# Kernel optimization log

Hardware: AMD Instinct MI355X
Metric: run time of the kernel (lower is better)

Reference implementation:

```python
import jax, jax.numpy as jnp
import numpy as np

# Circuit dimensions: B batch, N sum nodes (rows), C child nodes (cols), NSE stored edges.
B, N, C, NSE = 256, 8192, 32768, 524288


def setup_inputs() -> dict:
    key = jax.random.key(0)
    k1, k2, k3, k4 = jax.random.split(key, 4)
    # child log-likelihoods (output of child_layer.log_likelihood_of_nodes), [B, C]
    child_ll = jax.random.normal(k1, (B, C), dtype=jnp.float32) - 2.0
    # BCOO .data of the (unnormalized) log weights, [NSE]
    log_w_data = jax.random.normal(k2, (NSE,), dtype=jnp.float32)
    # BCOO indices[:, 0]: parent sum-node row of each edge. Guarantee every row
    # appears at least once so no node is empty (log(0) avoided), then sort
    # (matching .sort_indices() row-major ordering).
    rows = jnp.sort(jnp.concatenate([
        jnp.arange(N, dtype=jnp.int32),
        jax.random.randint(k3, (NSE - N,), 0, N, dtype=jnp.int32),
    ]))
    # BCOO indices[:, 1]: child node column of each edge
    cols = jax.random.randint(k4, (NSE,), 0, C, dtype=jnp.int32)
    return {"child_ll": child_ll, "log_w_data": log_w_data,
            "rows": rows, "cols": cols, "n_nodes": N}


def reference(child_ll, log_w_data, rows, cols, n_nodes):
    # log normalization constants per node (max-stabilized, as in
    # SparseSumLayer.log_normalization_constants)
    m = log_w_data.max()
    z = m + jnp.log(jax.ops.segment_sum(jnp.exp(log_w_data - m), rows,
                                        num_segments=n_nodes))  # [N]
    # per-edge: exp(log_w + child_ll[col])  (as in log_likelihood_of_nodes_single)
    vals = jnp.exp(log_w_data[None, :] + child_ll[:, cols])        # [B, NSE]
    # row-wise sparse sum (BCOO .sum(1).todense())
    summed = jax.ops.segment_sum(vals.T, rows, num_segments=n_nodes).T  # [B, N]
    # normalized log-likelihood of each sum node
    return jnp.log(summed) - z[None, :]
```

## Files before the change

kernel.cpp:

```cpp
#include <hip/hip_runtime.h>
#include <hip/hip_bf16.h>

#define BB   256
#define NN   8192
#define CC   32768
#define NSE_ 524288
#define GB   32
#define PREP_BLOCKS ((NSE_ + 64 + 255) / 256)
#define TP_BLOCKS   ((CC / 64) * 8)

typedef float v2f __attribute__((ext_vector_type(2)));

__device__ __forceinline__ unsigned int f2bf_rne(float f) {
    unsigned int u = __float_as_uint(f);
    return (u + 0x7fffu + ((u >> 16) & 1u)) >> 16;
}
__device__ __forceinline__ unsigned int pack2bf(float lo, float hi) {
    return f2bf_rne(lo) | (f2bf_rne(hi) << 16);
}

__global__ __launch_bounds__(256) void prep_transpose_kernel(
    const float* __restrict__ lw, const int* __restrict__ rows,
    const int* __restrict__ cols, const float* __restrict__ ll,
    uint2* __restrict__ cw, int* __restrict__ rs,
    unsigned int* __restrict__ cet32) {
    int bid = blockIdx.x;
    int t = threadIdx.x;
    if (bid < PREP_BLOCKS) {
        int e = bid * 256 + t;
        if (e < NSE_) {
            cw[e] = make_uint2((unsigned)cols[e],
                               __float_as_uint(__expf(lw[e])));
            if (e == 0) { rs[0] = 0; rs[NN] = NSE_; }
            else if (rows[e] != rows[e - 1]) rs[rows[e]] = e;
        } else if (e < NSE_ + 64) {
            cw[e] = make_uint2(0u, 0u);
        }
        return;
    }
    bid -= PREP_BLOCKS;
    int g = bid & 7;
    int ct = bid >> 3;
    int c0 = ct * 64, b0 = g * GB;
    __shared__ unsigned int tile_u[16][68];
    {
        int c4 = t & 15, bp = t >> 4;
        const float4 fa = *reinterpret_cast<const float4*>(
            ll + (size_t)(b0 + 2 * bp + 0) * CC + c0 + 4 * c4);
        const float4 fb = *reinterpret_cast<const float4*>(
            ll + (size_t)(b0 + 2 * bp + 1) * CC + c0 + 4 * c4);
        uint4 u;
        u.x = pack2bf(__expf(fa.x), __expf(fb.x));
        u.y = pack2bf(__expf(fa.y), __expf(fb.y));
        u.z = pack2bf(__expf(fa.z), __expf(fb.z));
        u.w = pack2bf(__expf(fa.w), __expf(fb.w));
        *reinterpret_cast<uint4*>(&tile_u[bp][4 * c4]) = u;
    }
    __syncthreads();
    {
        int c = t >> 2, q = t & 3;
        uint4 o;
        o.x = tile_u[4 * q + 0][c];
        o.y = tile_u[4 * q + 1][c];
        o.z = tile_u[4 * q + 2][c];
        o.w = tile_u[4 * q + 3][c];
        size_t base_u = ((size_t)g * CC + c0) * 16;
        *reinterpret_cast<uint4*>(cet32 + base_u + c * 16 + 4 * q) = o;
    }
}

__global__ __launch_bounds__(256) void sum_rows_kernel(
    const uint2* __restrict__ cw, const int* __restrict__ rs,
    const uint4* __restrict__ cet, float* __restrict__ out) {
    __shared__ uint2 stage[4][64];
    __shared__ float lds_out[32][17];
    int g = blockIdx.x & 7;
    int ntile = blockIdx.x >> 3;
    int n0 = ntile * 16;
    int wv = threadIdx.x >> 6;
    int lane = threadIdx.x & 63;
    int grp = lane >> 2;
    int bq = lane & 3;
    const uint4* slice = cet + (size_t)g * CC * 4;
    uint2* st = stage[wv];

    for (int r = 0; r < 4; ++r) {
        int n = n0 + wv * 4 + r;
        int s = __builtin_amdgcn_readfirstlane(rs[n]);
        int t = __builtin_amdgcn_readfirstlane(rs[n + 1]);
        v2f acc[4];
        acc[0] = 0.f; acc[1] = 0.f; acc[2] = 0.f; acc[3] = 0.f;
        float zs = 0.f;
        uint2 v = cw[s + lane];
        for (int eb = s; eb < t; eb += 64) {
            if (eb + lane >= t) v.y = 0u;
            st[lane] = v;
            if (eb + 64 < t) v = cw[eb + 64 + lane];
            #pragma unroll
            for (int j = 0; j < 4; ++j) {
                uint2 p = st[j * 16 + grp];
                float w = __uint_as_float(p.y);
                uint4 u = slice[(p.x << 2) | bq];
                v2f w2; w2.x = w; w2.y = w;
                v2f g0, g1, g2, g3;
                g0.x = __uint_as_float(u.x << 16);
                g0.y = __uint_as_float(u.x & 0xffff0000u);
                g1.x = __uint_as_float(u.y << 16);
                g1.y = __uint_as_float(u.y & 0xffff0000u);
                g2.x = __uint_as_float(u.z << 16);
                g2.y = __uint_as_float(u.z & 0xffff0000u);
                g3.x = __uint_as_float(u.w << 16);
                g3.y = __uint_as_float(u.w & 0xffff0000u);
                acc[0] += w2 * g0;
                acc[1] += w2 * g1;
                acc[2] += w2 * g2;
                acc[3] += w2 * g3;
                zs += w;
            }
        }
        #pragma unroll
        for (int off = 4; off <= 32; off <<= 1) {
            #pragma unroll
            for (int k = 0; k < 4; ++k) {
                acc[k].x += __shfl_xor(acc[k].x, off);
                acc[k].y += __shfl_xor(acc[k].y, off);
            }
            zs += __shfl_xor(zs, off);
        }
        if (grp == 0) {
            float lz = __logf(zs);
            #pragma unroll
            for (int k = 0; k < 4; ++k) {
                lds_out[bq * 8 + k * 2 + 0][wv * 4 + r] = __logf(acc[k].x) - lz;
                lds_out[bq * 8 + k * 2 + 1][wv * 4 + r] = __logf(acc[k].y) - lz;
            }
        }
    }
    __syncthreads();
    if (threadIdx.x < 128) {
        int bl = threadIdx.x >> 2, ch = threadIdx.x & 3;
        float4 v = make_float4(lds_out[bl][ch * 4 + 0], lds_out[bl][ch * 4 + 1],
                               lds_out[bl][ch * 4 + 2], lds_out[bl][ch * 4 + 3]);
        *reinterpret_cast<float4*>(
            out + (size_t)(g * GB + bl) * NN + n0 + ch * 4) = v;
    }
}

extern "C" void kernel_launch(void* const* d_in, const int* in_sizes, int n_in,
                              void* d_out, int out_size, void* d_ws, size_t ws_size,
                              hipStream_t stream) {
    const float* child_ll = (const float*)d_in[0];
    const float* log_w    = (const float*)d_in[1];
    const int*   rows     = (const int*)  d_in[2];
    const int*   cols     = (const int*)  d_in[3];
    float* out = (float*)d_out;

    char* ws = (char*)d_ws;
    uint2*        cwp = (uint2*)ws;
    int*          rs  = (int*)(ws + (size_t)6 * 1024 * 1024);
    unsigned int* cet = (unsigned int*)(ws + (size_t)8 * 1024 * 1024);

    prep_transpose_kernel<<<PREP_BLOCKS + TP_BLOCKS, 256, 0, stream>>>(
        log_w, rows, cols, child_ll, cwp, rs, cet);
    sum_rows_kernel<<<(NN / 16) * 8, 256, 0, stream>>>(
        cwp, rs, (const uint4*)cet, out);
}
```

Before: 128.1 us.

## Use persistent XCD-affine work stealing and interleave two rows per wave

Replaces the fixed block-to-(batch group, row tile) mapping with a persistent grid of 2048 blocks. Each block reads its XCD id and pulls row tiles through atomic counters, starting with the batch-group slice that matches its XCD so that slice stays hot in that XCD's L2. Each wave also processes two sum-node rows at once to expose more independent gathers. The costs are atomic and barrier overhead per tile, higher register pressure, and load imbalance when the two interleaved rows differ in length.

```diff
diff --git a/kernel.cpp b/kernel.cpp
--- a/kernel.cpp
+++ b/kernel.cpp
@@ -6,6 +6,7 @@
 #define CC   32768
 #define NSE_ 524288
 #define GB   32
+#define NTILES (NN / 16)
 #define PREP_BLOCKS ((NSE_ + 64 + 255) / 256)
 #define TP_BLOCKS   ((CC / 64) * 8)
 
@@ -23,10 +24,11 @@
     const float* __restrict__ lw, const int* __restrict__ rows,
     const int* __restrict__ cols, const float* __restrict__ ll,
     uint2* __restrict__ cw, int* __restrict__ rs,
-    unsigned int* __restrict__ cet32) {
+    unsigned int* __restrict__ cet32, int* __restrict__ cnt) {
     int bid = blockIdx.x;
     int t = threadIdx.x;
     if (bid < PREP_BLOCKS) {
+        if (bid == 0 && t < 8) cnt[t] = 0;
         int e = bid * 256 + t;
         if (e < NSE_) {
             cw[e] = make_uint2((unsigned)cols[e],
@@ -71,78 +73,126 @@
 
 __global__ __launch_bounds__(256) void sum_rows_kernel(
     const uint2* __restrict__ cw, const int* __restrict__ rs,
-    const uint4* __restrict__ cet, float* __restrict__ out) {
-    __shared__ uint2 stage[4][64];
+    const uint4* __restrict__ cet, int* __restrict__ cnt,
+    float* __restrict__ out) {
+    __shared__ uint2 stage[4][2][64];
     __shared__ float lds_out[32][17];
-    int g = blockIdx.x & 7;
-    int ntile = blockIdx.x >> 3;
-    int n0 = ntile * 16;
+    __shared__ int tile_sh;
     int wv = threadIdx.x >> 6;
     int lane = threadIdx.x & 63;
     int grp = lane >> 2;
     int bq = lane & 3;
-    const uint4* slice = cet + (size_t)g * CC * 4;
-    uint2* st = stage[wv];
-
-    for (int r = 0; r < 4; ++r) {
-        int n = n0 + wv * 4 + r;
-        int s = __builtin_amdgcn_readfirstlane(rs[n]);
-        int t = __builtin_amdgcn_readfirstlane(rs[n + 1]);
-        v2f acc[4];
-        acc[0] = 0.f; acc[1] = 0.f; acc[2] = 0.f; acc[3] = 0.f;
-        float zs = 0.f;
-        uint2 v = cw[s + lane];
-        for (int eb = s; eb < t; eb += 64) {
-            if (eb + lane >= t) v.y = 0u;
-            st[lane] = v;
-            if (eb + 64 < t) v = cw[eb + 64 + lane];
-            #pragma unroll
-            for (int j = 0; j < 4; ++j) {
-                uint2 p = st[j * 16 + grp];
-                float w = __uint_as_float(p.y);
-                uint4 u = slice[(p.x << 2) | bq];
-                v2f w2; w2.x = w; w2.y = w;
-                v2f g0, g1, g2, g3;
-                g0.x = __uint_as_float(u.x << 16);
-                g0.y = __uint_as_float(u.x & 0xffff0000u);
-                g1.x = __uint_as_float(u.y << 16);
-                g1.y = __uint_as_float(u.y & 0xffff0000u);
-                g2.x = __uint_as_float(u.z << 16);
-                g2.y = __uint_as_float(u.z & 0xffff0000u);
-                g3.x = __uint_as_float(u.w << 16);
-                g3.y = __uint_as_float(u.w & 0xffff0000u);
-                acc[0] += w2 * g0;
-                acc[1] += w2 * g1;
-                acc[2] += w2 * g2;
-                acc[3] += w2 * g3;
-                zs += w;
+    int xcd = __builtin_amdgcn_s_getreg(20 | (7 << 11)) & 7;
+
+    for (int k = 0; k < 8; ++k) {
+        int g = (xcd + k) & 7;
+        const uint4* slice = cet + (size_t)g * CC * 4;
+        for (;;) {
+            __syncthreads();
+            if (threadIdx.x == 0) tile_sh = atomicAdd(&cnt[g], 1);
+            __syncthreads();
+            int ntile = tile_sh;
+            if (ntile >= NTILES) break;
+            int n0 = ntile * 16;
+
+            for (int rp = 0; rp < 2; ++rp) {
+                int nA = n0 + wv * 4 + rp * 2;
+                int sA = __builtin_amdgcn_readfirstlane(rs[nA]);
+                int tA = __builtin_amdgcn_readfirstlane(rs[nA + 1]);
+                int sB = tA;
+                int tB = __builtin_amdgcn_readfirstlane(rs[nA + 2]);
+                v2f aA[4], aB[4];
+                aA[0] = 0.f; aA[1] = 0.f; aA[2] = 0.f; aA[3] = 0.f;
+                aB[0] = 0.f; aB[1] = 0.f; aB[2] = 0.f; aB[3] = 0.f;
+                float zA = 0.f, zB = 0.f;
+                uint2* stA = stage[wv][0];
+                uint2* stB = stage[wv][1];
+                uint2 vA = cw[sA + lane];
+                uint2 vB = cw[sB + lane];
+                int ebA = sA, ebB = sB;
+                while (ebA < tA || ebB < tB) {
+                    uint2 wA = vA, wB = vB;
+                    if (ebA + lane >= tA) wA.y = 0u;
+                    if (ebB + lane >= tB) wB.y = 0u;
+                    stA[lane] = wA;
+                    stB[lane] = wB;
+                    if (ebA + 64 < tA) vA = cw[ebA + 64 + lane];
+                    if (ebB + 64 < tB) vB = cw[ebB + 64 + lane];
+                    #pragma unroll
+                    for (int j = 0; j < 4; ++j) {
+                        uint2 pA = stA[j * 16 + grp];
+                        uint2 pB = stB[j * 16 + grp];
+                        uint4 uA = slice[(pA.x << 2) | bq];
+                        uint4 uB = slice[(pB.x << 2) | bq];
+                        float wa = __uint_as_float(pA.y);
+                        float wb = __uint_as_float(pB.y);
+                        v2f w2a; w2a.x = wa; w2a.y = wa;
+                        v2f w2b; w2b.x = wb; w2b.y = wb;
+                        v2f q0, q1, q2, q3;
+                        q0.x = __uint_as_float(uA.x << 16);
+                        q0.y = __uint_as_float(uA.x & 0xffff0000u);
+                        q1.x = __uint_as_float(uA.y << 16);
+                        q1.y = __uint_as_float(uA.y & 0xffff0000u);
+                        q2.x = __uint_as_float(uA.z << 16);
+                        q2.y = __uint_as_float(uA.z & 0xffff0000u);
+                        q3.x = __uint_as_float(uA.w << 16);
+                        q3.y = __uint_as_float(uA.w & 0xffff0000u);
+                        aA[0] += w2a * q0;
+                        aA[1] += w2a * q1;
+                        aA[2] += w2a * q2;
+                        aA[3] += w2a * q3;
+                        q0.x = __uint_as_float(uB.x << 16);
+                        q0.y = __uint_as_float(uB.x & 0xffff0000u);
+                        q1.x = __uint_as_float(uB.y << 16);
+                        q1.y = __uint_as_float(uB.y & 0xffff0000u);
+                        q2.x = __uint_as_float(uB.z << 16);
+                        q2.y = __uint_as_float(uB.z & 0xffff0000u);
+                        q3.x = __uint_as_float(uB.w << 16);
+                        q3.y = __uint_as_float(uB.w & 0xffff0000u);
+                        aB[0] += w2b * q0;
+                        aB[1] += w2b * q1;
+                        aB[2] += w2b * q2;
+                        aB[3] += w2b * q3;
+                        zA += wa;
+                        zB += wb;
+                    }
+                    ebA += 64;
+                    ebB += 64;
+                }
+                #pragma unroll
+                for (int off = 4; off <= 32; off <<= 1) {
+                    #pragma unroll
+                    for (int q = 0; q < 4; ++q) {
+                        aA[q].x += __shfl_xor(aA[q].x, off);
+                        aA[q].y += __shfl_xor(aA[q].y, off);
+                        aB[q].x += __shfl_xor(aB[q].x, off);
+                        aB[q].y += __shfl_xor(aB[q].y, off);
+                    }
+                    zA += __shfl_xor(zA, off);
+                    zB += __shfl_xor(zB, off);
+                }
+                if (grp == 0) {
+                    float lzA = __logf(zA), lzB = __logf(zB);
+                    int col = wv * 4 + rp * 2;
+                    #pragma unroll
+                    for (int q = 0; q < 4; ++q) {
+                        lds_out[bq * 8 + q * 2 + 0][col] = __logf(aA[q].x) - lzA;
+                        lds_out[bq * 8 + q * 2 + 1][col] = __logf(aA[q].y) - lzA;
+                        lds_out[bq * 8 + q * 2 + 0][col + 1] = __logf(aB[q].x) - lzB;
+                        lds_out[bq * 8 + q * 2 + 1][col + 1] = __logf(aB[q].y) - lzB;
+                    }
+                }
+            }
+            __syncthreads();
+            if (threadIdx.x < 128) {
+                int bl = threadIdx.x >> 2, ch = threadIdx.x & 3;
+                float4 v = make_float4(
+                    lds_out[bl][ch * 4 + 0], lds_out[bl][ch * 4 + 1],
+                    lds_out[bl][ch * 4 + 2], lds_out[bl][ch * 4 + 3]);
+                *reinterpret_cast<float4*>(
+                    out + (size_t)(g * GB + bl) * NN + n0 + ch * 4) = v;
             }
         }
-        #pragma unroll
-        for (int off = 4; off <= 32; off <<= 1) {
-            #pragma unroll
-            for (int k = 0; k < 4; ++k) {
-                acc[k].x += __shfl_xor(acc[k].x, off);
-                acc[k].y += __shfl_xor(acc[k].y, off);
-            }
-            zs += __shfl_xor(zs, off);
-        }
-        if (grp == 0) {
-            float lz = __logf(zs);
-            #pragma unroll
-            for (int k = 0; k < 4; ++k) {
-                lds_out[bq * 8 + k * 2 + 0][wv * 4 + r] = __logf(acc[k].x) - lz;
-                lds_out[bq * 8 + k * 2 + 1][wv * 4 + r] = __logf(acc[k].y) - lz;
-            }
-        }
-    }
-    __syncthreads();
-    if (threadIdx.x < 128) {
-        int bl = threadIdx.x >> 2, ch = threadIdx.x & 3;
-        float4 v = make_float4(lds_out[bl][ch * 4 + 0], lds_out[bl][ch * 4 + 1],
-                               lds_out[bl][ch * 4 + 2], lds_out[bl][ch * 4 + 3]);
-        *reinterpret_cast<float4*>(
-            out + (size_t)(g * GB + bl) * NN + n0 + ch * 4) = v;
     }
 }
 
@@ -158,10 +208,11 @@
     char* ws = (char*)d_ws;
     uint2*        cwp = (uint2*)ws;
     int*          rs  = (int*)(ws + (size_t)6 * 1024 * 1024);
+    int*          cnt = (int*)(ws + (size_t)7 * 1024 * 1024);
     unsigned int* cet = (unsigned int*)(ws + (size_t)8 * 1024 * 1024);
 
     prep_transpose_kernel<<<PREP_BLOCKS + TP_BLOCKS, 256, 0, stream>>>(
-        log_w, rows, cols, child_ll, cwp, rs, cet);
-    sum_rows_kernel<<<(NN / 16) * 8, 256, 0, stream>>>(
-        cwp, rs, (const uint4*)cet, out);
-}
+        log_w, rows, cols, child_ll, cwp, rs, cet, cnt);
+    sum_rows_kernel<<<2048, 256, 0, stream>>>(
+        cwp, rs, (const uint4*)cet, cnt, out);
+}
```

Result: slower. 337.3 us (+163.4%).

## Store exp child likelihoods as scaled FP8 and widen batch group to 64

Applied to the files above, without the earlier changes.

Converts the transposed exp(child_ll) table from bf16 to FP8, multiplied by a scale of 8 that is removed again in log space. Each 16-byte gather now yields 16 batch values instead of 8, so the batch group grows to 64 and the gather grid shrinks by half. This halves the random-gather traffic and the number of edge-list passes. In exchange, FP8 precision is much coarser, and small exp values can underflow, which risks accuracy failures.

```diff
diff --git a/kernel.cpp b/kernel.cpp
--- a/kernel.cpp
+++ b/kernel.cpp
@@ -5,25 +5,27 @@
 #define NN   8192
 #define CC   32768
 #define NSE_ 524288
-#define GB   32
+#define GB   64
 #define PREP_BLOCKS ((NSE_ + 64 + 255) / 256)
-#define TP_BLOCKS   ((CC / 64) * 8)
+#define TP_BLOCKS   ((CC / 64) * 4)
 
 typedef float v2f __attribute__((ext_vector_type(2)));
 
-__device__ __forceinline__ unsigned int f2bf_rne(float f) {
-    unsigned int u = __float_as_uint(f);
-    return (u + 0x7fffu + ((u >> 16) & 1u)) >> 16;
-}
-__device__ __forceinline__ unsigned int pack2bf(float lo, float hi) {
-    return f2bf_rne(lo) | (f2bf_rne(hi) << 16);
+#define FP8_SCALE  8.0f
+#define LOG_SCALE  2.0794415416798357f
+
+__device__ __forceinline__ unsigned int pack4_fp8(float a, float b, float c,
+                                                  float d) {
+    int v = __builtin_amdgcn_cvt_pk_fp8_f32(a, b, 0, false);
+    v = __builtin_amdgcn_cvt_pk_fp8_f32(c, d, v, true);
+    return (unsigned)v;
 }
 
 __global__ __launch_bounds__(256) void prep_transpose_kernel(
     const float* __restrict__ lw, const int* __restrict__ rows,
     const int* __restrict__ cols, const float* __restrict__ ll,
     uint2* __restrict__ cw, int* __restrict__ rs,
-    unsigned int* __restrict__ cet32) {
+    unsigned char* __restrict__ cet) {
     int bid = blockIdx.x;
     int t = threadIdx.x;
     if (bid < PREP_BLOCKS) {
@@ -39,33 +41,36 @@
         return;
     }
     bid -= PREP_BLOCKS;
-    int g = bid & 7;
-    int ct = bid >> 3;
+    int g = bid & 3;
+    int ct = bid >> 2;
     int c0 = ct * 64, b0 = g * GB;
-    __shared__ unsigned int tile_u[16][68];
-    {
-        int c4 = t & 15, bp = t >> 4;
-        const float4 fa = *reinterpret_cast<const float4*>(
-            ll + (size_t)(b0 + 2 * bp + 0) * CC + c0 + 4 * c4);
-        const float4 fb = *reinterpret_cast<const float4*>(
-            ll + (size_t)(b0 + 2 * bp + 1) * CC + c0 + 4 * c4);
-        uint4 u;
-        u.x = pack2bf(__expf(fa.x), __expf(fb.x));
-        u.y = pack2bf(__expf(fa.y), __expf(fb.y));
-        u.z = pack2bf(__expf(fa.z), __expf(fb.z));
-        u.w = pack2bf(__expf(fa.w), __expf(fb.w));
-        *reinterpret_cast<uint4*>(&tile_u[bp][4 * c4]) = u;
+    __shared__ float tile[64][65];
+    #pragma unroll
+    for (int k = 0; k < 4; ++k) {
+        int row = (t >> 4) + 16 * k;
+        int c4 = t & 15;
+        const float4 v = *reinterpret_cast<const float4*>(
+            ll + (size_t)(b0 + row) * CC + c0 + 4 * c4);
+        tile[c4 * 4 + 0][row] = v.x;
+        tile[c4 * 4 + 1][row] = v.y;
+        tile[c4 * 4 + 2][row] = v.z;
+        tile[c4 * 4 + 3][row] = v.w;
     }
     __syncthreads();
     {
-        int c = t >> 2, q = t & 3;
-        uint4 o;
-        o.x = tile_u[4 * q + 0][c];
-        o.y = tile_u[4 * q + 1][c];
-        o.z = tile_u[4 * q + 2][c];
-        o.w = tile_u[4 * q + 3][c];
-        size_t base_u = ((size_t)g * CC + c0) * 16;
-        *reinterpret_cast<uint4*>(cet32 + base_u + c * 16 + 4 * q) = o;
+        int cl = t >> 2, q = t & 3;
+        unsigned int o[4];
+        #pragma unroll
+        for (int i = 0; i < 4; ++i) {
+            int b = q * 16 + i * 4;
+            o[i] = pack4_fp8(__expf(tile[cl][b + 0]) * FP8_SCALE,
+                             __expf(tile[cl][b + 1]) * FP8_SCALE,
+                             __expf(tile[cl][b + 2]) * FP8_SCALE,
+                             __expf(tile[cl][b + 3]) * FP8_SCALE);
+        }
+        uint4 u4 = make_uint4(o[0], o[1], o[2], o[3]);
+        *reinterpret_cast<uint4*>(
+            cet + ((size_t)g * CC + c0 + cl) * GB + q * 16) = u4;
     }
 }
 
@@ -73,9 +78,9 @@
     const uint2* __restrict__ cw, const int* __restrict__ rs,
     const uint4* __restrict__ cet, float* __restrict__ out) {
     __shared__ uint2 stage[4][64];
-    __shared__ float lds_out[32][17];
-    int g = blockIdx.x & 7;
-    int ntile = blockIdx.x >> 3;
+    __shared__ float lds_out[64][17];
+    int g = blockIdx.x & 3;
+    int ntile = blockIdx.x >> 2;
     int n0 = ntile * 16;
     int wv = threadIdx.x >> 6;
     int lane = threadIdx.x & 63;
@@ -88,8 +93,9 @@
         int n = n0 + wv * 4 + r;
         int s = __builtin_amdgcn_readfirstlane(rs[n]);
         int t = __builtin_amdgcn_readfirstlane(rs[n + 1]);
-        v2f acc[4];
-        acc[0] = 0.f; acc[1] = 0.f; acc[2] = 0.f; acc[3] = 0.f;
+        v2f acc[8];
+        #pragma unroll
+        for (int k = 0; k < 8; ++k) acc[k] = 0.f;
         float zs = 0.f;
         uint2 v = cw[s + lane];
         for (int eb = s; eb < t; eb += 64) {
@@ -102,47 +108,43 @@
                 float w = __uint_as_float(p.y);
                 uint4 u = slice[(p.x << 2) | bq];
                 v2f w2; w2.x = w; w2.y = w;
-                v2f g0, g1, g2, g3;
-                g0.x = __uint_as_float(u.x << 16);
-                g0.y = __uint_as_float(u.x & 0xffff0000u);
-                g1.x = __uint_as_float(u.y << 16);
-                g1.y = __uint_as_float(u.y & 0xffff0000u);
-                g2.x = __uint_as_float(u.z << 16);
-                g2.y = __uint_as_float(u.z & 0xffff0000u);
-                g3.x = __uint_as_float(u.w << 16);
-                g3.y = __uint_as_float(u.w & 0xffff0000u);
-                acc[0] += w2 * g0;
-                acc[1] += w2 * g1;
-                acc[2] += w2 * g2;
-                acc[3] += w2 * g3;
+                acc[0] += w2 * __builtin_amdgcn_cvt_pk_f32_fp8(u.x, false);
+                acc[1] += w2 * __builtin_amdgcn_cvt_pk_f32_fp8(u.x, true);
+                acc[2] += w2 * __builtin_amdgcn_cvt_pk_f32_fp8(u.y, false);
+                acc[3] += w2 * __builtin_amdgcn_cvt_pk_f32_fp8(u.y, true);
+                acc[4] += w2 * __builtin_amdgcn_cvt_pk_f32_fp8(u.z, false);
+                acc[5] += w2 * __builtin_amdgcn_cvt_pk_f32_fp8(u.z, true);
+                acc[6] += w2 * __builtin_amdgcn_cvt_pk_f32_fp8(u.w, false);
+                acc[7] += w2 * __builtin_amdgcn_cvt_pk_f32_fp8(u.w, true);
                 zs += w;
             }
         }
         #pragma unroll
         for (int off = 4; off <= 32; off <<= 1) {
             #pragma unroll
-            for (int k = 0; k < 4; ++k) {
+            for (int k = 0; k < 8; ++k) {
                 acc[k].x += __shfl_xor(acc[k].x, off);
                 acc[k].y += __shfl_xor(acc[k].y, off);
             }
             zs += __shfl_xor(zs, off);
         }
         if (grp == 0) {
-            float lz = __logf(zs);
+            float lz = __logf(zs) + LOG_SCALE;
+            int col = wv * 4 + r;
             #pragma unroll
-            for (int k = 0; k < 4; ++k) {
-                lds_out[bq * 8 + k * 2 + 0][wv * 4 + r] = __logf(acc[k].x) - lz;
-                lds_out[bq * 8 + k * 2 + 1][wv * 4 + r] = __logf(acc[k].y) - lz;
+            for (int k = 0; k < 8; ++k) {
+                lds_out[bq * 16 + 2 * k + 0][col] = __logf(acc[k].x) - lz;
+                lds_out[bq * 16 + 2 * k + 1][col] = __logf(acc[k].y) - lz;
             }
         }
     }
     __syncthreads();
-    if (threadIdx.x < 128) {
+    {
         int bl = threadIdx.x >> 2, ch = threadIdx.x & 3;
-        float4 v = make_float4(lds_out[bl][ch * 4 + 0], lds_out[bl][ch * 4 + 1],
+        float4 o = make_float4(lds_out[bl][ch * 4 + 0], lds_out[bl][ch * 4 + 1],
                                lds_out[bl][ch * 4 + 2], lds_out[bl][ch * 4 + 3]);
         *reinterpret_cast<float4*>(
-            out + (size_t)(g * GB + bl) * NN + n0 + ch * 4) = v;
+            out + (size_t)(g * GB + bl) * NN + n0 + ch * 4) = o;
     }
 }
 
@@ -156,12 +158,12 @@
     float* out = (float*)d_out;
 
     char* ws = (char*)d_ws;
-    uint2*        cwp = (uint2*)ws;
-    int*          rs  = (int*)(ws + (size_t)6 * 1024 * 1024);
-    unsigned int* cet = (unsigned int*)(ws + (size_t)8 * 1024 * 1024);
+    uint2*         cwp = (uint2*)ws;
+    int*           rs  = (int*)(ws + (size_t)5 * 1024 * 1024);
+    unsigned char* cet = (unsigned char*)(ws + (size_t)6 * 1024 * 1024);
 
     prep_transpose_kernel<<<PREP_BLOCKS + TP_BLOCKS, 256, 0, stream>>>(
         log_w, rows, cols, child_ll, cwp, rs, cet);
-    sum_rows_kernel<<<(NN / 16) * 8, 256, 0, stream>>>(
+    sum_rows_kernel<<<(NN / 16) * 4, 256, 0, stream>>>(
         cwp, rs, (const uint4*)cet, out);
 }
```

New measurement: 125.3 us. -2.2%, faster.
